# Optimization experiments

Measured on AMD Instinct MI355X. Metric: run time of the kernel, lower is better.

## Reference

```python
import jax, jax.numpy as jnp
import numpy as np
from jax import lax


def setup_inputs() -> dict:
    key = jax.random.key(0)
    ks = jax.random.split(key, 12)
    B, T = 64, 256
    H, EN, ET, D = 512, 256, 256, 256  # hidden, embN, embT, embT_dyn (==ET since embedding_sizeT_dyn=None)
    VN, VT, VS = 300, 1000, 100       # vocab_sizeN, vocab_sizeT, num static ids (static_x_ids = range(100))
    s = 0.05
    ar = jnp.arange(VT)
    inp = {}
    inp["n_input"] = jax.random.randint(ks[0], (B, T), 0, VN)
    inp["t_input"] = jax.random.randint(ks[1], (B, T), 0, VT)
    inp["is_static_vocab"] = ar < VS                      # membership test (t in static_x_ids)
    inp["static2dense"] = jnp.where(ar < VS, ar, 0)       # static id -> row in embeddingT
    inp["dynamic2dense"] = jnp.where(ar >= VS, ar - VS, 0)  # dynamic id -> dense dynamic slot
    inp["embN"] = jax.random.normal(ks[2], (VN, EN)) * s
    inp["embT"] = jax.random.normal(ks[3], (VS, ET)) * s
    inp["W_ih"] = jax.random.normal(ks[4], (4 * H, EN + ET)) * s
    inp["W_hh"] = jax.random.normal(ks[5], (4 * H, H)) * s
    inp["b_ih"] = jax.random.normal(ks[6], (4 * H,)) * s
    inp["b_hh"] = jax.random.normal(ks[7], (4 * H,)) * s
    inp["Wd_ih"] = jax.random.normal(ks[8], (4 * D, EN + H)) * s
    inp["Wd_hh"] = jax.random.normal(ks[9], (4 * D, D)) * s
    inp["bd_ih"] = jax.random.normal(ks[10], (4 * D,)) * s
    inp["bd_hh"] = jax.random.normal(ks[11], (4 * D,)) * s
    inp["hid_init"] = jnp.zeros((H,))
    inp["cell_init"] = jnp.zeros((H,))
    inp["dyn_init_h"] = jnp.zeros((1, D))  # anonym_type='pure_zeros'
    inp["dyn_init_c"] = jnp.zeros((1, D))
    return inp


def _lstm_cell(x, h, c, Wi, Wh, bi, bh):
    # torch.nn.LSTMCell gate order: i, f, g, o
    g = x @ Wi.T + bi + h @ Wh.T + bh
    i, f, gg, o = jnp.split(g, 4, axis=-1)
    c2 = jax.nn.sigmoid(f) * c + jax.nn.sigmoid(i) * jnp.tanh(gg)
    return jax.nn.sigmoid(o) * jnp.tanh(c2), c2


def reference(n_input, t_input, is_static_vocab, static2dense, dynamic2dense,
              embN, embT, W_ih, W_hh, b_ih, b_hh,
              Wd_ih, Wd_hh, bd_ih, bd_hh,
              hid_init, cell_init, dyn_init_h, dyn_init_c):
    # The torch module's growing (lookup_table, de_h, de_c) cache is equivalent to
    # per-(batch, dynamic-token) state arrays Hd/Cd [B, V_dyn, D] with a 'seen' flag:
    # each (b, token) pair owns exactly one cache slot that is read/updated in place.
    B, T = n_input.shape
    H = hid_init.shape[0]
    D = dyn_init_h.shape[-1]
    VD = int(dynamic2dense.max()) + 1  # number of dynamic vocab slots (static at setup)
    bidx = jnp.arange(B)
    init_h = jnp.broadcast_to(dyn_init_h, (B, D))
    init_c = jnp.broadcast_to(dyn_init_c, (B, D))

    def step(carry, xt):
        h, c, seen, Hd, Cd = carry
        nt, tt = xt
        is_st = is_static_vocab[tt]            # [B] bool
        didx = dynamic2dense[tt]               # [B] dynamic slot (garbage 0 for static rows, masked below)
        sn = seen[bidx, didx]                  # was this (b, token) created before?
        hd_prev = jnp.where(sn[:, None], Hd[bidx, didx], init_h)
        cd_prev = jnp.where(sn[:, None], Cd[bidx, didx], init_c)
        n_emb = embN[nt]                       # [B, EN] (dropout=0 -> plain lookup)
        # emb_transform is identity (embedding_sizeT_dyn is None)
        h_tensor = jnp.where(is_st[:, None], embT[static2dense[tt]], hd_prev)  # [B, ET]
        h_new, c_new = _lstm_cell(jnp.concatenate([n_emb, h_tensor], 1), h, c, W_ih, W_hh, b_ih, b_hh)
        # dynamic-embedding LSTM: input is (n_emb, previous main hidden h)
        hd_new, cd_new = _lstm_cell(jnp.concatenate([n_emb, h], 1), hd_prev, cd_prev, Wd_ih, Wd_hh, bd_ih, bd_hh)
        dyn = (~is_st)[:, None]
        Hd = Hd.at[bidx, didx].set(jnp.where(dyn, hd_new, Hd[bidx, didx]))
        Cd = Cd.at[bidx, didx].set(jnp.where(dyn, cd_new, Cd[bidx, didx]))
        seen = seen.at[bidx, didx].set(sn | (~is_st))
        return (h_new, c_new, seen, Hd, Cd), h_new

    h0 = jnp.broadcast_to(hid_init, (B, H)) + 0.0
    c0 = jnp.broadcast_to(cell_init, (B, H)) + 0.0
    carry0 = (h0, c0,
              jnp.zeros((B, VD), dtype=bool),
              jnp.zeros((B, VD, D), dtype=embN.dtype),
              jnp.zeros((B, VD, D), dtype=embN.dtype))
    _, outs = lax.scan(step, carry0, (n_input.T, t_input.T))  # outs: [T, B, H]
    return jnp.transpose(outs, (1, 0, 2))                     # [B, T, H]
```

## Files before the change

### kernel.cpp

```cpp
#include <hip/hip_runtime.h>


typedef _Float16 f16;
typedef _Float16 f16x8 __attribute__((ext_vector_type(8)));
typedef float f32x4 __attribute__((ext_vector_type(4)));

#define B_ 64
#define T_ 256
#define H_ 512
#define EN_ 256
#define ET_ 256
#define D_ 256
#define VN_ 300
#define VS_ 100

#define NB_MAIN_ 128
#define NB_DYN_ 64
#define NBLK_ 192
#define NTHR_ 256
#define NSH_ 64
#define PER_SHARD_ (NBLK_ / NSH_)
#define POLL_CAP_ (1u << 22)

static constexpr size_t OFF_CNT  = 0;
static constexpr size_t OFF_EMBN = 4096;
static constexpr size_t OFF_EMBT = OFF_EMBN + (size_t)VN_ * EN_ * 2;
static constexpr size_t OFF_DINH = OFF_EMBT + (size_t)VS_ * ET_ * 2;
static constexpr size_t OFF_PREV = OFF_DINH + 1024;
static constexpr size_t OFF_HH   = OFF_PREV + (size_t)T_ * B_ * 4;
static constexpr size_t OFF_HD   = OFF_HH + (size_t)(T_ + 1) * B_ * H_ * 2;
static constexpr size_t OFF_CD   = OFF_HD + (size_t)T_ * B_ * D_ * 2;
static constexpr size_t WS_NEED  = OFF_CD + (size_t)T_ * B_ * D_ * 4;

struct RnnParams {
  const int* n_input; const int* t_input; const int* s2d;
  const float* W_ih; const float* W_hh; const float* b_ih; const float* b_hh;
  const float* Wd_ih; const float* Wd_hh; const float* bd_ih; const float* bd_hh;
  const float* cell_init; const float* dyn_init_c;
  const f16* embN16; const f16* embT16; const f16* dynih16;
  const int* prev;
  f16* Hhist; f16* HdHist; float* CdHist;
  float* out; unsigned* cnt;
};

__device__ __forceinline__ float sigm(float x) { return 1.f / (1.f + __expf(-x)); }
__device__ __forceinline__ float tanh_fast(float x) {
  float e = __expf(2.f * x);
  return 1.f - 2.f / (e + 1.f);
}

__device__ __forceinline__ void cstore8(void* p, unsigned long long v) {
  __hip_atomic_store((unsigned long long*)p, v, __ATOMIC_RELAXED,
                     __HIP_MEMORY_SCOPE_AGENT);
}
__device__ __forceinline__ void cstore16(void* p, f32x4 v) {
  asm volatile("global_store_dwordx4 %0, %1, off sc0 sc1"
               :: "v"(p), "v"(v) : "memory");
}

__global__ void setup_kernel(const float* embN, const float* embT,
                             const float* hid_init, const float* dyn_init_h,
                             f16* embN16, f16* embT16, f16* dynih16,
                             f16* Hhist0, unsigned* cnt) {
  int i = blockIdx.x * blockDim.x + threadIdx.x;
  if (i < 1024)      cnt[i] = 0u;
  if (i < VN_ * EN_) embN16[i] = (f16)embN[i];
  if (i < VS_ * ET_) embT16[i] = (f16)embT[i];
  if (i < D_)        dynih16[i] = (f16)dyn_init_h[i];
  if (i < B_ * H_)   Hhist0[i] = (f16)hid_init[i & (H_ - 1)];
  __threadfence();
}

__global__ void prev_kernel(const int* t_input, const int* s2d, int* prev) {
  int idx = blockIdx.x * blockDim.x + threadIdx.x;
  if (idx < B_ * T_) {
    int b = idx / T_, t = idx % T_;
    int tt = t_input[b * T_ + t];
    int p = -1;
    if (s2d[tt] != tt) {
      for (int q = t - 1; q >= 0; --q)
        if (t_input[b * T_ + q] == tt) { p = q; break; }
    }
    prev[t * B_ + b] = p;
  }
  __threadfence();
}

__device__ __forceinline__ void resolve(const RnnParams& p, bool isDyn, int t, int b,
                                        int tprev,
                                        const f16** aN, const f16** aX,
                                        const float** aC, int* dynw, int* rc) {
  const int nt = p.n_input[b * T_ + t];
  aN[b] = p.embN16 + (size_t)nt * EN_;
  const int tt = p.t_input[b * T_ + t];
  const int pv = p.prev[t * B_ + b];
  rc[b] = (pv >= 0 && pv == tprev) ? 1 : 0;
  const f16* hd = (pv >= 0) ? (p.HdHist + ((size_t)pv * B_ + b) * D_) : p.dynih16;
  const int s2 = p.s2d[tt];
  const bool st = (s2 == tt);
  if (!isDyn) {
    aX[b] = st ? (p.embT16 + (size_t)s2 * ET_) : hd;
  } else {
    aX[b] = hd;
    aC[b] = (pv >= 0) ? (p.CdHist + ((size_t)pv * B_ + b) * D_) : p.dyn_init_c;
    dynw[b] = st ? 0 : 1;
  }
}

__global__ __launch_bounds__(NTHR_, 1) void rnn_main(RnnParams p) {
  const int blk  = blockIdx.x;
  const int tid  = threadIdx.x;
  const int wave = tid >> 6;
  const int lane = tid & 63;
  const bool isDyn = (blk >= NB_MAIN_);
  const int u0 = isDyn ? (blk - NB_MAIN_) * 4 : blk * 4;

  __threadfence();

  __shared__ float s_bias[16];
  __shared__ float s_scr[64][17];
  __shared__ const f16*  s_aN[2][64];
  __shared__ const f16*  s_aX[2][64];
  __shared__ const float* s_aC[2][64];
  __shared__ int s_dynw[2][64];
  __shared__ int s_rc[2][64];

  const int nIdx = lane & 15;
  const int ui = nIdx & 3, gate = nIdx >> 2;
  const int ko = (lane >> 4) * 8;
  f16x8 w[32];
  if (!isDyn) {
    const int r = gate * H_ + u0 + ui;
#pragma unroll
    for (int s = 0; s < 32; ++s) {
      const int k = s * 32 + ko;
      const float* src = (k < 512) ? (p.W_ih + (size_t)r * 512 + k)
                                   : (p.W_hh + (size_t)r * 512 + (k - 512));
      f16x8 v;
#pragma unroll
      for (int j = 0; j < 8; ++j) v[j] = (f16)src[j];
      w[s] = v;
    }
  } else {
    const int r = gate * D_ + u0 + ui;
#pragma unroll
    for (int s = 0; s < 32; ++s) {
      const int k = s * 32 + ko;
      const float* src = (k < 768) ? (p.Wd_ih + (size_t)r * 768 + k)
                                   : (p.Wd_hh + (size_t)r * 256 + (k - 768));
      f16x8 v;
#pragma unroll
      for (int j = 0; j < 8; ++j) v[j] = (f16)src[j];
      w[s] = v;
    }
  }
  if (tid < 16) {
    int g2 = tid >> 2, un2 = tid & 3;
    s_bias[tid] = isDyn ? (p.bd_ih[g2 * D_ + u0 + un2] + p.bd_hh[g2 * D_ + u0 + un2])
                        : (p.b_ih[g2 * H_ + u0 + un2] + p.b_hh[g2 * H_ + u0 + un2]);
  }
  float creg[4] = {0.f, 0.f, 0.f, 0.f};
  if (tid < 64 && !isDyn) {
#pragma unroll
    for (int un = 0; un < 4; ++un) creg[un] = p.cell_init[u0 + un];
  }
  if (tid < 64)
    resolve(p, isDyn, 0, tid, -1, s_aN[0], s_aX[0], s_aC[0], s_dynw[0], s_rc[0]);
  __syncthreads();

  const int b = (wave << 4) + (lane & 15);
  f16x8 pf[16];
  float4 cvp = {0.f, 0.f, 0.f, 0.f};
  {
    const f16* pN = s_aN[0][b];
    const f16* pX = s_aX[0][b];
#pragma unroll
    for (int i = 0; i < 8; ++i) pf[i] = *(const f16x8*)(pN + i * 32 + ko);
#pragma unroll
    for (int i = 0; i < 8; ++i) pf[8 + i] = *(const f16x8*)(pX + i * 32 + ko);
    if (isDyn && tid < 64) cvp = *(const float4*)(s_aC[0][tid] + u0);
  }

  for (int t = 0; t < T_; ++t) {
    const int pb = t & 1;

    const f16* pH = p.Hhist + ((size_t)t * B_ + b) * H_;
    f16x8 hh[16];
#pragma unroll
    for (int i = 0; i < 16; ++i) hh[i] = *(const f16x8*)(pH + i * 32 + ko);
    if (s_rc[pb][b]) {
      const f16* pX = s_aX[pb][b];
#pragma unroll
      for (int i = 0; i < 8; ++i) pf[8 + i] = *(const f16x8*)(pX + i * 32 + ko);
    }

    f32x4 ac[4] = {{0,0,0,0},{0,0,0,0},{0,0,0,0},{0,0,0,0}};
    if (!isDyn) {
#pragma unroll
      for (int i = 0; i < 8; ++i)
        ac[i & 3] = __builtin_amdgcn_mfma_f32_16x16x32_f16(pf[i], w[i], ac[i & 3], 0, 0, 0);
#pragma unroll
      for (int i = 0; i < 8; ++i)
        ac[i & 3] = __builtin_amdgcn_mfma_f32_16x16x32_f16(pf[8 + i], w[8 + i], ac[i & 3], 0, 0, 0);
#pragma unroll
      for (int i = 0; i < 16; ++i)
        ac[i & 3] = __builtin_amdgcn_mfma_f32_16x16x32_f16(hh[i], w[16 + i], ac[i & 3], 0, 0, 0);
    } else {
#pragma unroll
      for (int i = 0; i < 8; ++i)
        ac[i & 3] = __builtin_amdgcn_mfma_f32_16x16x32_f16(pf[i], w[i], ac[i & 3], 0, 0, 0);
#pragma unroll
      for (int i = 0; i < 8; ++i)
        ac[i & 3] = __builtin_amdgcn_mfma_f32_16x16x32_f16(pf[8 + i], w[24 + i], ac[i & 3], 0, 0, 0);
#pragma unroll
      for (int i = 0; i < 16; ++i)
        ac[i & 3] = __builtin_amdgcn_mfma_f32_16x16x32_f16(hh[i], w[8 + i], ac[i & 3], 0, 0, 0);
    }
    f32x4 acc = (ac[0] + ac[1]) + (ac[2] + ac[3]);
#pragma unroll
    for (int j = 0; j < 4; ++j)
      s_scr[(wave << 4) + ((lane >> 4) << 2) + j][lane & 15] = acc[j];
    __syncthreads();

    if (tid < 64) {
      const int eb = tid;
      if (isDyn && s_rc[pb][eb])
        cvp = *(const float4*)(s_aC[pb][eb] + u0);
      float g[16];
#pragma unroll
      for (int n = 0; n < 16; ++n) g[n] = s_scr[eb][n] + s_bias[n];
      if (!isDyn) {
        float4 ho;
        union { f16 h[4]; unsigned long long u; } pk;
#pragma unroll
        for (int un = 0; un < 4; ++un) {
          float c = sigm(g[4 + un]) * creg[un] + sigm(g[un]) * tanh_fast(g[8 + un]);
          creg[un] = c;
          float h = sigm(g[12 + un]) * tanh_fast(c);
          (&ho.x)[un] = h;
          pk.h[un] = (f16)h;
        }
        *(float4*)&p.out[((size_t)eb * T_ + t) * H_ + u0] = ho;
        cstore8(&p.Hhist[((size_t)(t + 1) * B_ + eb) * H_ + u0], pk.u);
      } else {
        const float cold[4] = {cvp.x, cvp.y, cvp.z, cvp.w};
        f32x4 co;
        union { f16 h[4]; unsigned long long u; } pk;
#pragma unroll
        for (int un = 0; un < 4; ++un) {
          float c = sigm(g[4 + un]) * cold[un] + sigm(g[un]) * tanh_fast(g[8 + un]);
          float h = sigm(g[12 + un]) * tanh_fast(c);
          pk.h[un] = (f16)h;
          co[un] = c;
        }
        if (s_dynw[pb][eb]) {
          cstore8(&p.HdHist[((size_t)t * B_ + eb) * D_ + u0], pk.u);
          cstore16(&p.CdHist[((size_t)t * B_ + eb) * D_ + u0], co);
        }
      }
    } else if (tid < 128 && t + 1 < T_) {
      resolve(p, isDyn, t + 1, tid - 64, t,
              s_aN[pb ^ 1], s_aX[pb ^ 1], s_aC[pb ^ 1], s_dynw[pb ^ 1], s_rc[pb ^ 1]);
    }

    if (t + 1 < T_) {
      __syncthreads();
      if (tid == 0)
        __hip_atomic_fetch_add(&p.cnt[(blk & (NSH_ - 1)) << 4], 1u,
                               __ATOMIC_RELAXED, __HIP_MEMORY_SCOPE_AGENT);
      {
        const f16* pN2 = s_aN[pb ^ 1][b];
        const f16* pX2 = s_aX[pb ^ 1][b];
#pragma unroll
        for (int i = 0; i < 8; ++i) pf[i] = *(const f16x8*)(pN2 + i * 32 + ko);
#pragma unroll
        for (int i = 0; i < 8; ++i) pf[8 + i] = *(const f16x8*)(pX2 + i * 32 + ko);
        if (isDyn && tid < 64) cvp = *(const float4*)(s_aC[pb ^ 1][tid] + u0);
      }
      if (tid < NSH_) {
        const unsigned tgt = (unsigned)(t + 1) * PER_SHARD_;
        unsigned it = 0;
        while (__hip_atomic_load(&p.cnt[tid << 4], __ATOMIC_RELAXED,
                                 __HIP_MEMORY_SCOPE_AGENT) < tgt &&
               ++it < POLL_CAP_)
          __builtin_amdgcn_s_sleep(1);
      }
      __syncthreads();
    }
  }
}

extern "C" void kernel_launch(void* const* d_in, const int* in_sizes, int n_in,
                              void* d_out, int out_size, void* d_ws, size_t ws_size,
                              hipStream_t stream) {
  (void)in_sizes; (void)n_in; (void)out_size;
  const int* n_input   = (const int*)d_in[0];
  const int* t_input   = (const int*)d_in[1];
  const int* s2d       = (const int*)d_in[3];
  const float* embN    = (const float*)d_in[5];
  const float* embT    = (const float*)d_in[6];
  const float* W_ih    = (const float*)d_in[7];
  const float* W_hh    = (const float*)d_in[8];
  const float* b_ih    = (const float*)d_in[9];
  const float* b_hh    = (const float*)d_in[10];
  const float* Wd_ih   = (const float*)d_in[11];
  const float* Wd_hh   = (const float*)d_in[12];
  const float* bd_ih   = (const float*)d_in[13];
  const float* bd_hh   = (const float*)d_in[14];
  const float* hid_init  = (const float*)d_in[15];
  const float* cell_init = (const float*)d_in[16];
  const float* dyn_init_h = (const float*)d_in[17];
  const float* dyn_init_c = (const float*)d_in[18];

  char* ws = (char*)d_ws;
  unsigned* cnt  = (unsigned*)(ws + OFF_CNT);
  f16* embN16    = (f16*)(ws + OFF_EMBN);
  f16* embT16    = (f16*)(ws + OFF_EMBT);
  f16* dynih16   = (f16*)(ws + OFF_DINH);
  int* prev      = (int*)(ws + OFF_PREV);
  f16* Hhist     = (f16*)(ws + OFF_HH);
  f16* HdHist    = (f16*)(ws + OFF_HD);
  float* CdHist  = (float*)(ws + OFF_CD);
  if (ws_size < WS_NEED) return;

  setup_kernel<<<dim3((VN_ * EN_ + NTHR_ - 1) / NTHR_), dim3(NTHR_), 0, stream>>>(
      embN, embT, hid_init, dyn_init_h, embN16, embT16, dynih16, Hhist, cnt);
  prev_kernel<<<dim3((B_ * T_ + NTHR_ - 1) / NTHR_), dim3(NTHR_), 0, stream>>>(
      t_input, s2d, prev);

  RnnParams prm;
  prm.n_input = n_input; prm.t_input = t_input; prm.s2d = s2d;
  prm.W_ih = W_ih; prm.W_hh = W_hh; prm.b_ih = b_ih; prm.b_hh = b_hh;
  prm.Wd_ih = Wd_ih; prm.Wd_hh = Wd_hh; prm.bd_ih = bd_ih; prm.bd_hh = bd_hh;
  prm.cell_init = cell_init; prm.dyn_init_c = dyn_init_c;
  prm.embN16 = embN16; prm.embT16 = embT16; prm.dynih16 = dynih16;
  prm.prev = prev; prm.Hhist = Hhist; prm.HdHist = HdHist; prm.CdHist = CdHist;
  prm.out = (float*)d_out; prm.cnt = cnt;

  void* args[] = { &prm };
  hipError_t e = hipLaunchCooperativeKernel((const void*)rnn_main,
                                            dim3(NBLK_), dim3(NTHR_), args, 0, stream);
  if (e != hipSuccess) {
    rnn_main<<<dim3(NBLK_), dim3(NTHR_), 0, stream>>>(prm);
  }
}
```

Measured before the change: 1.397 ms.

## Replace global all-block barrier with per-step producer/consumer flag counters

Replaces the sharded grid-wide barrier with per-timestep ready counters. Main blocks signal that H(t+1) is ready, dynamic blocks signal that their HdHist/CdHist writes for step t are done, and consumers poll only the counter they depend on. Dynamic-history reads switch to coherent sc0 sc1 loads and are guarded by wave-level any-checks, so the waits happen only when a recurrence read is needed. This lets main and dynamic blocks drift relative to each other instead of lockstepping. The cost is more counter words and polls inside the loop, plus subtler memory-ordering correctness.

```diff
diff --git a/kernel.cpp b/kernel.cpp
--- a/kernel.cpp
+++ b/kernel.cpp
@@ -18,12 +18,14 @@
 #define NB_DYN_ 64
 #define NBLK_ 192
 #define NTHR_ 256
-#define NSH_ 64
-#define PER_SHARD_ (NBLK_ / NSH_)
 #define POLL_CAP_ (1u << 22)
 
+#define IDXW_HRDY(t) ((unsigned)(t) << 4)
+#define IDXW_DNER(t) ((unsigned)(260 + (t)) << 4)
+#define CNT_WORDS_ 8448
+
 static constexpr size_t OFF_CNT  = 0;
-static constexpr size_t OFF_EMBN = 4096;
+static constexpr size_t OFF_EMBN = 64 * 1024;
 static constexpr size_t OFF_EMBT = OFF_EMBN + (size_t)VN_ * EN_ * 2;
 static constexpr size_t OFF_DINH = OFF_EMBT + (size_t)VS_ * ET_ * 2;
 static constexpr size_t OFF_PREV = OFF_DINH + 1024;
@@ -57,13 +59,34 @@
   asm volatile("global_store_dwordx4 %0, %1, off sc0 sc1"
                :: "v"(p), "v"(v) : "memory");
 }
+__device__ __forceinline__ f16x8 scload16(const f16* p) {
+  f16x8 v;
+  asm volatile("global_load_dwordx4 %0, %1, off sc0 sc1\n\ts_waitcnt vmcnt(0)"
+               : "=&v"(v) : "v"(p) : "memory");
+  return v;
+}
+__device__ __forceinline__ float4 scload16f(const float* p) {
+  float4 v;
+  asm volatile("global_load_dwordx4 %0, %1, off sc0 sc1\n\ts_waitcnt vmcnt(0)"
+               : "=&v"(v) : "v"(p) : "memory");
+  return v;
+}
+__device__ __forceinline__ void poll_ge(unsigned* w, unsigned tgt) {
+  unsigned it = 0;
+  while (__hip_atomic_load(w, __ATOMIC_RELAXED, __HIP_MEMORY_SCOPE_AGENT) < tgt &&
+         ++it < POLL_CAP_)
+    __builtin_amdgcn_s_sleep(1);
+}
+__device__ __forceinline__ void lds_barrier() {
+  asm volatile("s_waitcnt lgkmcnt(0)\n\ts_barrier" ::: "memory");
+}
 
 __global__ void setup_kernel(const float* embN, const float* embT,
                              const float* hid_init, const float* dyn_init_h,
                              f16* embN16, f16* embT16, f16* dynih16,
                              f16* Hhist0, unsigned* cnt) {
   int i = blockIdx.x * blockDim.x + threadIdx.x;
-  if (i < 1024)      cnt[i] = 0u;
+  if (i < CNT_WORDS_) cnt[i] = (i == 0) ? 128u : 0u;
   if (i < VN_ * EN_) embN16[i] = (f16)embN[i];
   if (i < VS_ * ET_) embT16[i] = (f16)embT[i];
   if (i < D_)        dynih16[i] = (f16)dyn_init_h[i];
@@ -184,14 +207,20 @@
   for (int t = 0; t < T_; ++t) {
     const int pb = t & 1;
 
+    poll_ge(&p.cnt[IDXW_HRDY(t)], 128u);
     const f16* pH = p.Hhist + ((size_t)t * B_ + b) * H_;
     f16x8 hh[16];
 #pragma unroll
     for (int i = 0; i < 16; ++i) hh[i] = *(const f16x8*)(pH + i * 32 + ko);
-    if (s_rc[pb][b]) {
-      const f16* pX = s_aX[pb][b];
-#pragma unroll
-      for (int i = 0; i < 8; ++i) pf[8 + i] = *(const f16x8*)(pX + i * 32 + ko);
+
+    const bool need = (s_rc[pb][b] != 0);
+    if (__any(need)) {
+      if (t >= 1) poll_ge(&p.cnt[IDXW_DNER(t - 1)], 64u);
+      if (need) {
+        const f16* pX = s_aX[pb][b];
+#pragma unroll
+        for (int i = 0; i < 8; ++i) pf[8 + i] = scload16(pX + i * 32 + ko);
+      }
     }
 
     f32x4 ac[4] = {{0,0,0,0},{0,0,0,0},{0,0,0,0},{0,0,0,0}};
@@ -220,12 +249,17 @@
 #pragma unroll
     for (int j = 0; j < 4; ++j)
       s_scr[(wave << 4) + ((lane >> 4) << 2) + j][lane & 15] = acc[j];
-    __syncthreads();
+    lds_barrier();
 
     if (tid < 64) {
       const int eb = tid;
-      if (isDyn && s_rc[pb][eb])
-        cvp = *(const float4*)(s_aC[pb][eb] + u0);
+      if (isDyn) {
+        const bool cneed = (s_rc[pb][eb] != 0);
+        if (__any(cneed)) {
+          if (t >= 1) poll_ge(&p.cnt[IDXW_DNER(t - 1)], 64u);
+          if (cneed) cvp = scload16f(s_aC[pb][eb] + u0);
+        }
+      }
       float g[16];
 #pragma unroll
       for (int n = 0; n < 16; ++n) g[n] = s_scr[eb][n] + s_bias[n];
@@ -262,30 +296,26 @@
       resolve(p, isDyn, t + 1, tid - 64, t,
               s_aN[pb ^ 1], s_aX[pb ^ 1], s_aC[pb ^ 1], s_dynw[pb ^ 1], s_rc[pb ^ 1]);
     }
+    lds_barrier();
+
+    if (t + 1 < T_ || isDyn) {
+      if (tid < 64) {
+        asm volatile("s_waitcnt vmcnt(0)" ::: "memory");
+        if (tid == 0)
+          __hip_atomic_fetch_add(&p.cnt[isDyn ? IDXW_DNER(t) : IDXW_HRDY(t + 1)],
+                                 1u, __ATOMIC_RELAXED, __HIP_MEMORY_SCOPE_AGENT);
+      }
+    }
 
     if (t + 1 < T_) {
-      __syncthreads();
-      if (tid == 0)
-        __hip_atomic_fetch_add(&p.cnt[(blk & (NSH_ - 1)) << 4], 1u,
-                               __ATOMIC_RELAXED, __HIP_MEMORY_SCOPE_AGENT);
-      {
-        const f16* pN2 = s_aN[pb ^ 1][b];
-        const f16* pX2 = s_aX[pb ^ 1][b];
-#pragma unroll
-        for (int i = 0; i < 8; ++i) pf[i] = *(const f16x8*)(pN2 + i * 32 + ko);
-#pragma unroll
-        for (int i = 0; i < 8; ++i) pf[8 + i] = *(const f16x8*)(pX2 + i * 32 + ko);
-        if (isDyn && tid < 64) cvp = *(const float4*)(s_aC[pb ^ 1][tid] + u0);
-      }
-      if (tid < NSH_) {
-        const unsigned tgt = (unsigned)(t + 1) * PER_SHARD_;
-        unsigned it = 0;
-        while (__hip_atomic_load(&p.cnt[tid << 4], __ATOMIC_RELAXED,
-                                 __HIP_MEMORY_SCOPE_AGENT) < tgt &&
-               ++it < POLL_CAP_)
-          __builtin_amdgcn_s_sleep(1);
-      }
-      __syncthreads();
+      if (t >= 1) poll_ge(&p.cnt[IDXW_DNER(t - 1)], 64u);
+      const f16* pN2 = s_aN[pb ^ 1][b];
+      const f16* pX2 = s_aX[pb ^ 1][b];
+#pragma unroll
+      for (int i = 0; i < 8; ++i) pf[i] = *(const f16x8*)(pN2 + i * 32 + ko);
+#pragma unroll
+      for (int i = 0; i < 8; ++i) pf[8 + i] = *(const f16x8*)(pX2 + i * 32 + ko);
+      if (isDyn && tid < 64) cvp = *(const float4*)(s_aC[pb ^ 1][tid] + u0);
     }
   }
 }
```

After: 1.920 ms. 37.4% more time.

## Replace global barrier with split main/dynamic counters and per-wave dependency polling

Applied to the files above, without the earlier changes.

Removes the full all-block barrier at the end of each timestep and replaces it with two groups of counters, one for main blocks and one for dynamic blocks. Each wave polls only for the dependencies it actually needs: main hidden state from the previous step and dynamic state with a lag. Per-step index resolution moves from shared memory into registers, the LDS scratch buffer is double-buffered, and the block-wide syncthreads calls become a lighter lds barrier. This lets main and dynamic blocks drift apart and overlap across steps, at the cost of subtle memory-ordering correctness that depends on the relaxed atomics and cache-bypassing loads.

```diff
diff --git a/kernel.cpp b/kernel.cpp
--- a/kernel.cpp
+++ b/kernel.cpp
@@ -18,9 +18,9 @@
 #define NB_DYN_ 64
 #define NBLK_ 192
 #define NTHR_ 256
-#define NSH_ 64
-#define PER_SHARD_ (NBLK_ / NSH_)
 #define POLL_CAP_ (1u << 22)
+
+#define DNER_W_ 512
 
 static constexpr size_t OFF_CNT  = 0;
 static constexpr size_t OFF_EMBN = 4096;
@@ -56,6 +56,32 @@
 __device__ __forceinline__ void cstore16(void* p, f32x4 v) {
   asm volatile("global_store_dwordx4 %0, %1, off sc0 sc1"
                :: "v"(p), "v"(v) : "memory");
+}
+__device__ __forceinline__ float4 scload16f(const float* p) {
+  float4 v;
+  asm volatile("global_load_dwordx4 %0, %1, off sc0 sc1\n\ts_waitcnt vmcnt(0)"
+               : "=&v"(v) : "v"(p) : "memory");
+  return v;
+}
+__device__ __forceinline__ unsigned cld(const unsigned* w) {
+  return __hip_atomic_load(w, __ATOMIC_RELAXED, __HIP_MEMORY_SCOPE_AGENT);
+}
+__device__ __forceinline__ void poll_main(const unsigned* cnt, int lane,
+                                          unsigned ht, unsigned dt) {
+  const unsigned* w; unsigned tgt;
+  if (lane < 16)      { w = cnt + (lane << 4);                 tgt = ht; }
+  else if (lane < 32) { w = cnt + DNER_W_ + ((lane - 16) << 4); tgt = dt; }
+  else                { w = cnt;                                tgt = 0u; }
+  unsigned it = 0;
+  while (__any(cld(w) < tgt) && ++it < POLL_CAP_) __builtin_amdgcn_s_sleep(1);
+}
+__device__ __forceinline__ void poll_dner(const unsigned* cnt, int lane, unsigned tgt) {
+  const unsigned* w = cnt + DNER_W_ + ((lane & 15) << 4);
+  unsigned it = 0;
+  while (__any(cld(w) < tgt) && ++it < POLL_CAP_) __builtin_amdgcn_s_sleep(1);
+}
+__device__ __forceinline__ void lds_barrier() {
+  asm volatile("s_waitcnt lgkmcnt(0)\n\ts_barrier" ::: "memory");
 }
 
 __global__ void setup_kernel(const float* embN, const float* embT,
@@ -86,27 +112,6 @@
   __threadfence();
 }
 
-__device__ __forceinline__ void resolve(const RnnParams& p, bool isDyn, int t, int b,
-                                        int tprev,
-                                        const f16** aN, const f16** aX,
-                                        const float** aC, int* dynw, int* rc) {
-  const int nt = p.n_input[b * T_ + t];
-  aN[b] = p.embN16 + (size_t)nt * EN_;
-  const int tt = p.t_input[b * T_ + t];
-  const int pv = p.prev[t * B_ + b];
-  rc[b] = (pv >= 0 && pv == tprev) ? 1 : 0;
-  const f16* hd = (pv >= 0) ? (p.HdHist + ((size_t)pv * B_ + b) * D_) : p.dynih16;
-  const int s2 = p.s2d[tt];
-  const bool st = (s2 == tt);
-  if (!isDyn) {
-    aX[b] = st ? (p.embT16 + (size_t)s2 * ET_) : hd;
-  } else {
-    aX[b] = hd;
-    aC[b] = (pv >= 0) ? (p.CdHist + ((size_t)pv * B_ + b) * D_) : p.dyn_init_c;
-    dynw[b] = st ? 0 : 1;
-  }
-}
-
 __global__ __launch_bounds__(NTHR_, 1) void rnn_main(RnnParams p) {
   const int blk  = blockIdx.x;
   const int tid  = threadIdx.x;
@@ -117,13 +122,7 @@
 
   __threadfence();
 
-  __shared__ float s_bias[16];
-  __shared__ float s_scr[64][17];
-  __shared__ const f16*  s_aN[2][64];
-  __shared__ const f16*  s_aX[2][64];
-  __shared__ const float* s_aC[2][64];
-  __shared__ int s_dynw[2][64];
-  __shared__ int s_rc[2][64];
+  __shared__ float s_scr[2][64][17];
 
   const int nIdx = lane & 15;
   const int ui = nIdx & 3, gate = nIdx >> 2;
@@ -154,44 +153,73 @@
       w[s] = v;
     }
   }
-  if (tid < 16) {
-    int g2 = tid >> 2, un2 = tid & 3;
-    s_bias[tid] = isDyn ? (p.bd_ih[g2 * D_ + u0 + un2] + p.bd_hh[g2 * D_ + u0 + un2])
-                        : (p.b_ih[g2 * H_ + u0 + un2] + p.b_hh[g2 * H_ + u0 + un2]);
-  }
-  float creg[4] = {0.f, 0.f, 0.f, 0.f};
-  if (tid < 64 && !isDyn) {
-#pragma unroll
-    for (int un = 0; un < 4; ++un) creg[un] = p.cell_init[u0 + un];
-  }
-  if (tid < 64)
-    resolve(p, isDyn, 0, tid, -1, s_aN[0], s_aX[0], s_aC[0], s_dynw[0], s_rc[0]);
-  __syncthreads();
+
+  float bias[16], creg[4] = {0.f, 0.f, 0.f, 0.f};
+  const float* aCe = p.dyn_init_c; int dynwE = 0, rcE = 0;
+  float4 cvp = {0.f, 0.f, 0.f, 0.f};
+  if (tid < 64) {
+#pragma unroll
+    for (int n = 0; n < 16; ++n) {
+      int gt = n >> 2, un = n & 3;
+      bias[n] = isDyn ? (p.bd_ih[gt * D_ + u0 + un] + p.bd_hh[gt * D_ + u0 + un])
+                      : (p.b_ih[gt * H_ + u0 + un] + p.b_hh[gt * H_ + u0 + un]);
+    }
+    if (!isDyn) {
+#pragma unroll
+      for (int un = 0; un < 4; ++un) creg[un] = p.cell_init[u0 + un];
+    } else {
+      const int eb = tid;
+      const int tt = p.t_input[eb * T_ + 0];
+      const int pv = p.prev[0 * B_ + eb];
+      dynwE = (p.s2d[tt] == tt) ? 0 : 1;
+      aCe = (pv >= 0) ? (p.CdHist + ((size_t)pv * B_ + eb) * D_) : p.dyn_init_c;
+      rcE = (pv >= 0 && pv + 1 >= 0) ? 1 : 0;
+      cvp = *(const float4*)(aCe + u0);
+    }
+  }
 
   const int b = (wave << 4) + (lane & 15);
+  const f16 *pN, *pX; int rc;
+  {
+    const int nt = p.n_input[b * T_ + 0];
+    pN = p.embN16 + (size_t)nt * EN_;
+    const int tt = p.t_input[b * T_ + 0];
+    const int pv = p.prev[0 * B_ + b];
+    const f16* hd = (pv >= 0) ? (p.HdHist + ((size_t)pv * B_ + b) * D_) : p.dynih16;
+    const int s2 = p.s2d[tt];
+    pX = (!isDyn && s2 == tt) ? (p.embT16 + (size_t)s2 * ET_) : hd;
+    rc = (pv >= 0 && pv + 2 >= 0) ? 1 : 0;
+  }
   f16x8 pf[16];
-  float4 cvp = {0.f, 0.f, 0.f, 0.f};
-  {
-    const f16* pN = s_aN[0][b];
-    const f16* pX = s_aX[0][b];
-#pragma unroll
-    for (int i = 0; i < 8; ++i) pf[i] = *(const f16x8*)(pN + i * 32 + ko);
-#pragma unroll
-    for (int i = 0; i < 8; ++i) pf[8 + i] = *(const f16x8*)(pX + i * 32 + ko);
-    if (isDyn && tid < 64) cvp = *(const float4*)(s_aC[0][tid] + u0);
-  }
+#pragma unroll
+  for (int i = 0; i < 8; ++i) pf[i] = *(const f16x8*)(pN + i * 32 + ko);
+#pragma unroll
+  for (int i = 0; i < 8; ++i) pf[8 + i] = *(const f16x8*)(pX + i * 32 + ko);
 
   for (int t = 0; t < T_; ++t) {
     const int pb = t & 1;
 
+    {
+      const unsigned ht = 8u * (unsigned)t;
+      const int dti = 4 * (t - 1);
+      poll_main(p.cnt, lane, ht, dti > 0 ? (unsigned)dti : 0u);
+    }
+
     const f16* pH = p.Hhist + ((size_t)t * B_ + b) * H_;
     f16x8 hh[16];
 #pragma unroll
     for (int i = 0; i < 16; ++i) hh[i] = *(const f16x8*)(pH + i * 32 + ko);
-    if (s_rc[pb][b]) {
-      const f16* pX = s_aX[pb][b];
-#pragma unroll
-      for (int i = 0; i < 8; ++i) pf[8 + i] = *(const f16x8*)(pX + i * 32 + ko);
+
+    if (__any(rc)) {
+      poll_dner(p.cnt, lane, 4u * (unsigned)t);
+      if (rc) {
+#pragma unroll
+        for (int i = 0; i < 8; ++i)
+          asm volatile("global_load_dwordx4 %0, %1, off sc0 sc1"
+                       : "=&v"(pf[8 + i]) : "v"(pX + i * 32 + ko));
+      }
+      asm volatile("s_waitcnt vmcnt(0)" ::: "memory");
+      __builtin_amdgcn_sched_barrier(0);
     }
 
     f32x4 ac[4] = {{0,0,0,0},{0,0,0,0},{0,0,0,0},{0,0,0,0}};
@@ -219,16 +247,18 @@
     f32x4 acc = (ac[0] + ac[1]) + (ac[2] + ac[3]);
 #pragma unroll
     for (int j = 0; j < 4; ++j)
-      s_scr[(wave << 4) + ((lane >> 4) << 2) + j][lane & 15] = acc[j];
-    __syncthreads();
+      s_scr[pb][(wave << 4) + ((lane >> 4) << 2) + j][lane & 15] = acc[j];
+    lds_barrier();
 
     if (tid < 64) {
       const int eb = tid;
-      if (isDyn && s_rc[pb][eb])
-        cvp = *(const float4*)(s_aC[pb][eb] + u0);
+      if (isDyn && __any(rcE)) {
+        poll_dner(p.cnt, lane, 4u * (unsigned)t);
+        if (rcE) cvp = scload16f(aCe + u0);
+      }
       float g[16];
 #pragma unroll
-      for (int n = 0; n < 16; ++n) g[n] = s_scr[eb][n] + s_bias[n];
+      for (int n = 0; n < 16; ++n) g[n] = s_scr[pb][eb][n] + bias[n];
       if (!isDyn) {
         float4 ho;
         union { f16 h[4]; unsigned long long u; } pk;
@@ -253,39 +283,47 @@
           pk.h[un] = (f16)h;
           co[un] = c;
         }
-        if (s_dynw[pb][eb]) {
+        if (dynwE) {
           cstore8(&p.HdHist[((size_t)t * B_ + eb) * D_ + u0], pk.u);
           cstore16(&p.CdHist[((size_t)t * B_ + eb) * D_ + u0], co);
         }
       }
-    } else if (tid < 128 && t + 1 < T_) {
-      resolve(p, isDyn, t + 1, tid - 64, t,
-              s_aN[pb ^ 1], s_aX[pb ^ 1], s_aC[pb ^ 1], s_dynw[pb ^ 1], s_rc[pb ^ 1]);
+      if (t + 1 < T_) {
+        asm volatile("s_waitcnt vmcnt(0)" ::: "memory");
+        if (lane == 0) {
+          const unsigned wd = isDyn ? (DNER_W_ + (((unsigned)(blk - NB_MAIN_)) & 15u) * 16u)
+                                    : ((((unsigned)blk) & 15u) * 16u);
+          __hip_atomic_fetch_add(&p.cnt[wd], 1u, __ATOMIC_RELAXED,
+                                 __HIP_MEMORY_SCOPE_AGENT);
+        }
+      }
     }
 
     if (t + 1 < T_) {
-      __syncthreads();
-      if (tid == 0)
-        __hip_atomic_fetch_add(&p.cnt[(blk & (NSH_ - 1)) << 4], 1u,
-                               __ATOMIC_RELAXED, __HIP_MEMORY_SCOPE_AGENT);
+      const int s = t + 1;
       {
-        const f16* pN2 = s_aN[pb ^ 1][b];
-        const f16* pX2 = s_aX[pb ^ 1][b];
-#pragma unroll
-        for (int i = 0; i < 8; ++i) pf[i] = *(const f16x8*)(pN2 + i * 32 + ko);
-#pragma unroll
-        for (int i = 0; i < 8; ++i) pf[8 + i] = *(const f16x8*)(pX2 + i * 32 + ko);
-        if (isDyn && tid < 64) cvp = *(const float4*)(s_aC[pb ^ 1][tid] + u0);
-      }
-      if (tid < NSH_) {
-        const unsigned tgt = (unsigned)(t + 1) * PER_SHARD_;
-        unsigned it = 0;
-        while (__hip_atomic_load(&p.cnt[tid << 4], __ATOMIC_RELAXED,
-                                 __HIP_MEMORY_SCOPE_AGENT) < tgt &&
-               ++it < POLL_CAP_)
-          __builtin_amdgcn_s_sleep(1);
-      }
-      __syncthreads();
+        const int nt = p.n_input[b * T_ + s];
+        pN = p.embN16 + (size_t)nt * EN_;
+        const int tt = p.t_input[b * T_ + s];
+        const int pv = p.prev[s * B_ + b];
+        const f16* hd = (pv >= 0) ? (p.HdHist + ((size_t)pv * B_ + b) * D_) : p.dynih16;
+        const int s2 = p.s2d[tt];
+        pX = (!isDyn && s2 == tt) ? (p.embT16 + (size_t)s2 * ET_) : hd;
+        rc = (pv >= 0 && pv + 2 >= s) ? 1 : 0;
+      }
+#pragma unroll
+      for (int i = 0; i < 8; ++i) pf[i] = *(const f16x8*)(pN + i * 32 + ko);
+#pragma unroll
+      for (int i = 0; i < 8; ++i) pf[8 + i] = *(const f16x8*)(pX + i * 32 + ko);
+      if (isDyn && tid < 64) {
+        const int eb = tid;
+        const int tt = p.t_input[eb * T_ + s];
+        const int pv = p.prev[s * B_ + eb];
+        dynwE = (p.s2d[tt] == tt) ? 0 : 1;
+        aCe = (pv >= 0) ? (p.CdHist + ((size_t)pv * B_ + eb) * D_) : p.dyn_init_c;
+        rcE = (pv >= 0 && pv + 1 >= s) ? 1 : 0;
+        cvp = *(const float4*)(aCe + u0);
+      }
     }
   }
 }
```

Result: slower. 2.014 ms (+44.1%).

## Retile hidden-state history for coalesced loads and lighten per-step barriers

Applied to the files above, without the earlier changes.

Stores the per-step hidden history in an interleaved layout so each wave's MFMA operand loads are contiguous 16-byte chunks across lanes. Makes the recurrent input reload conditional on any lane needing it and routes it through cache-bypassing loads, and does the same for the dynamic cell reload. Replaces __syncthreads with LDS-only waitcnt barriers and moves polling to a separate wave so the arrival signal and the spin loop do not serialize in one wave. It relies on hand-written waitcnt ordering for global stores before the counter increment, which risks subtle memory ordering issues.

```diff
diff --git a/kernel.cpp b/kernel.cpp
--- a/kernel.cpp
+++ b/kernel.cpp
@@ -57,6 +57,15 @@
   asm volatile("global_store_dwordx4 %0, %1, off sc0 sc1"
                :: "v"(p), "v"(v) : "memory");
 }
+__device__ __forceinline__ float4 scload16f(const float* p) {
+  float4 v;
+  asm volatile("global_load_dwordx4 %0, %1, off sc0 sc1\n\ts_waitcnt vmcnt(0)"
+               : "=&v"(v) : "v"(p) : "memory");
+  return v;
+}
+__device__ __forceinline__ void lds_barrier() {
+  asm volatile("s_waitcnt lgkmcnt(0)\n\ts_barrier" ::: "memory");
+}
 
 __global__ void setup_kernel(const float* embN, const float* embT,
                              const float* hid_init, const float* dyn_init_h,
@@ -67,7 +76,10 @@
   if (i < VN_ * EN_) embN16[i] = (f16)embN[i];
   if (i < VS_ * ET_) embT16[i] = (f16)embT[i];
   if (i < D_)        dynih16[i] = (f16)dyn_init_h[i];
-  if (i < B_ * H_)   Hhist0[i] = (f16)hid_init[i & (H_ - 1)];
+  if (i < B_ * H_) {
+    int b = i >> 9, k = i & 511;
+    Hhist0[(k >> 3) * 512 + b * 8 + (k & 7)] = (f16)hid_init[k];
+  }
   __threadfence();
 }
 
@@ -180,18 +192,29 @@
     for (int i = 0; i < 8; ++i) pf[8 + i] = *(const f16x8*)(pX + i * 32 + ko);
     if (isDyn && tid < 64) cvp = *(const float4*)(s_aC[0][tid] + u0);
   }
+  const int hoff = ((lane >> 4) << 9) + ((lane & 15) << 3) + (wave << 7);
 
   for (int t = 0; t < T_; ++t) {
     const int pb = t & 1;
 
-    const f16* pH = p.Hhist + ((size_t)t * B_ + b) * H_;
+    const f16* pH2 = p.Hhist + (size_t)t * 32768 + hoff;
     f16x8 hh[16];
 #pragma unroll
-    for (int i = 0; i < 16; ++i) hh[i] = *(const f16x8*)(pH + i * 32 + ko);
-    if (s_rc[pb][b]) {
-      const f16* pX = s_aX[pb][b];
-#pragma unroll
-      for (int i = 0; i < 8; ++i) pf[8 + i] = *(const f16x8*)(pX + i * 32 + ko);
+    for (int i = 0; i < 16; ++i) hh[i] = *(const f16x8*)(pH2 + i * 2048);
+
+    {
+      const int need = s_rc[pb][b];
+      if (__any(need)) {
+        if (need) {
+          const f16* pX = s_aX[pb][b];
+#pragma unroll
+          for (int i = 0; i < 8; ++i)
+            asm volatile("global_load_dwordx4 %0, %1, off sc0 sc1"
+                         : "=&v"(pf[8 + i]) : "v"(pX + i * 32 + ko));
+        }
+        asm volatile("s_waitcnt vmcnt(0)" ::: "memory");
+        __builtin_amdgcn_sched_barrier(0);
+      }
     }
 
     f32x4 ac[4] = {{0,0,0,0},{0,0,0,0},{0,0,0,0},{0,0,0,0}};
@@ -220,12 +243,17 @@
 #pragma unroll
     for (int j = 0; j < 4; ++j)
       s_scr[(wave << 4) + ((lane >> 4) << 2) + j][lane & 15] = acc[j];
-    __syncthreads();
+    lds_barrier();
 
     if (tid < 64) {
       const int eb = tid;
-      if (isDyn && s_rc[pb][eb])
-        cvp = *(const float4*)(s_aC[pb][eb] + u0);
+      if (isDyn) {
+        const int cneed = s_rc[pb][eb];
+        if (__any(cneed)) {
+          if (cneed) cvp = scload16f(s_aC[pb][eb] + u0);
+          __builtin_amdgcn_sched_barrier(0);
+        }
+      }
       float g[16];
 #pragma unroll
       for (int n = 0; n < 16; ++n) g[n] = s_scr[eb][n] + s_bias[n];
@@ -241,7 +269,8 @@
           pk.h[un] = (f16)h;
         }
         *(float4*)&p.out[((size_t)eb * T_ + t) * H_ + u0] = ho;
-        cstore8(&p.Hhist[((size_t)(t + 1) * B_ + eb) * H_ + u0], pk.u);
+        cstore8(&p.Hhist[(size_t)(t + 1) * 32768 + (size_t)(u0 >> 3) * 512
+                         + (size_t)eb * 8 + ((u0 >> 2) & 1) * 4], pk.u);
       } else {
         const float cold[4] = {cvp.x, cvp.y, cvp.z, cvp.w};
         f32x4 co;
@@ -262,12 +291,15 @@
       resolve(p, isDyn, t + 1, tid - 64, t,
               s_aN[pb ^ 1], s_aX[pb ^ 1], s_aC[pb ^ 1], s_dynw[pb ^ 1], s_rc[pb ^ 1]);
     }
+    lds_barrier();
 
     if (t + 1 < T_) {
-      __syncthreads();
-      if (tid == 0)
-        __hip_atomic_fetch_add(&p.cnt[(blk & (NSH_ - 1)) << 4], 1u,
-                               __ATOMIC_RELAXED, __HIP_MEMORY_SCOPE_AGENT);
+      if (wave == 0) {
+        asm volatile("s_waitcnt vmcnt(0)" ::: "memory");
+        if (tid == 0)
+          __hip_atomic_fetch_add(&p.cnt[(blk & (NSH_ - 1)) << 4], 1u,
+                                 __ATOMIC_RELAXED, __HIP_MEMORY_SCOPE_AGENT);
+      }
       {
         const f16* pN2 = s_aN[pb ^ 1][b];
         const f16* pX2 = s_aX[pb ^ 1][b];
@@ -277,15 +309,15 @@
         for (int i = 0; i < 8; ++i) pf[8 + i] = *(const f16x8*)(pX2 + i * 32 + ko);
         if (isDyn && tid < 64) cvp = *(const float4*)(s_aC[pb ^ 1][tid] + u0);
       }
-      if (tid < NSH_) {
+      if (wave == 1) {
         const unsigned tgt = (unsigned)(t + 1) * PER_SHARD_;
         unsigned it = 0;
-        while (__hip_atomic_load(&p.cnt[tid << 4], __ATOMIC_RELAXED,
+        while (__hip_atomic_load(&p.cnt[lane << 4], __ATOMIC_RELAXED,
                                  __HIP_MEMORY_SCOPE_AGENT) < tgt &&
                ++it < POLL_CAP_)
           __builtin_amdgcn_s_sleep(1);
       }
-      __syncthreads();
+      lds_barrier();
     }
   }
 }
```

Result: faster. 1.217 ms (-12.9%).
